# Optimization experiments

Hardware: AMD Instinct MI355X
Metric: run time of the kernel (lower is better)

The kernel has to match this reference:

```python
import jax, jax.numpy as jnp
import numpy as np

B, T, S, C, E, H = 4, 2048, 2048, 256, 512, 8
D = E // H
SCALE = E ** (-0.5)


def setup_inputs() -> dict:
    key = jax.random.key(0)
    ks = jax.random.split(key, 12)
    x = jax.random.normal(ks[0], (B, T, C), dtype=jnp.float32)
    context = jax.random.normal(ks[1], (B, S, E), dtype=jnp.float32)
    pad_mask = jax.random.randint(ks[2], (B, T, S), 0, 2) == 1
    p = 0.02
    # Conv1d kernel_size=1 weights stored squeezed: [out_ch, in_ch]
    w_in = jax.random.normal(ks[3], (E, C), dtype=jnp.float32) * p
    b_in = jnp.zeros((E,), dtype=jnp.float32)
    wq = jax.random.normal(ks[4], (E, E), dtype=jnp.float32) * p
    bq = jnp.zeros((E,), dtype=jnp.float32)
    wk = jax.random.normal(ks[5], (E, E), dtype=jnp.float32) * p
    bk = jnp.zeros((E,), dtype=jnp.float32)
    wv = jax.random.normal(ks[6], (E, E), dtype=jnp.float32) * p
    bv = jnp.zeros((E,), dtype=jnp.float32)
    w_out = jax.random.normal(ks[7], (C, E), dtype=jnp.float32) * p
    b_out = jnp.zeros((C,), dtype=jnp.float32)
    return {"x": x, "context": context, "pad_mask": pad_mask,
            "w_in": w_in, "b_in": b_in, "wq": wq, "bq": bq,
            "wk": wk, "bk": bk, "wv": wv, "bv": bv,
            "w_out": w_out, "b_out": b_out}


def reference(x, context, pad_mask, w_in, b_in, wq, bq, wk, bk, wv, bv, w_out, b_out):
    # proj_in: Conv1d k=1 == per-token linear on channel dim. [B,T,C] -> [B,T,E]
    xe = jnp.einsum('btc,ec->bte', x, w_in) + b_in
    Q = (xe @ wq.T + bq).reshape(B, T, H, D)       # query tokens
    K = (context @ wk.T + bk).reshape(B, S, H, D)  # key tokens
    V = (context @ wv.T + bv).reshape(B, S, H, D)
    att = jnp.einsum('bihd,bjhd->bhij', Q, K) * SCALE  # [B,H,T,S]
    att = jnp.where(pad_mask[:, None, :, :], jnp.float32(-1e9), att)
    att = jax.nn.softmax(att, axis=-1)
    out = jnp.einsum('bhij,bjhd->bihd', att, V).reshape(B, T, E)
    # proj_out: Conv1d k=1, [B,T,E] -> [B,T,C]
    out = jnp.einsum('bte,ce->btc', out, w_out) + b_out
    return out
```

## Files before the change

### kernel.cpp

```cpp
#include <hip/hip_runtime.h>
#include <cstdint>
#include <cstddef>

#define Bb 4
#define Tt 2048
#define Ssz 2048
#define Cc 256
#define Ee 512
#define Hh 8

typedef short bf8 __attribute__((ext_vector_type(8)));
typedef float f4 __attribute__((ext_vector_type(4)));
typedef float f16v __attribute__((ext_vector_type(16)));
typedef unsigned int u32x2 __attribute__((ext_vector_type(2)));
typedef unsigned int u32x4 __attribute__((ext_vector_type(4)));

__device__ __forceinline__ unsigned short f2bf(float x) {
  unsigned int u = __float_as_uint(x);
  u += 0x7fffu + ((u >> 16) & 1u);
  return (unsigned short)(u >> 16);
}

__device__ __forceinline__ bf8 cvt8(float4 a, float4 b) {
  bf8 r;
  r[0] = (short)f2bf(a.x); r[1] = (short)f2bf(a.y);
  r[2] = (short)f2bf(a.z); r[3] = (short)f2bf(a.w);
  r[4] = (short)f2bf(b.x); r[5] = (short)f2bf(b.y);
  r[6] = (short)f2bf(b.z); r[7] = (short)f2bf(b.w);
  return r;
}

#if __has_builtin(__builtin_amdgcn_perm)
#define PACK2(u0, u1) __builtin_amdgcn_perm((u1), (u0), 0x07060302u)
#else
#define PACK2(u0, u1) (((u0) >> 16) | ((u1) & 0xffff0000u))
#endif

#define EXPU(v) __float_as_uint(__builtin_amdgcn_exp2f(v))
#define MFMA32(a, b, c) __builtin_amdgcn_mfma_f32_32x32x16_bf16((a), (b), (c), 0, 0, 0)

__device__ __forceinline__ void pl32swap(unsigned int& a, unsigned int& b) {
#if __has_builtin(__builtin_amdgcn_permlane32_swap)
  u32x2 r = __builtin_amdgcn_permlane32_swap(a, b, false, false);
  a = r[0];
  b = r[1];
#else
  unsigned int ax = (unsigned int)__shfl_xor((int)a, 32);
  unsigned int bx = (unsigned int)__shfl_xor((int)b, 32);
  bool hi = (threadIdx.x & 32) != 0;
  unsigned int an = hi ? bx : a;
  unsigned int bn = hi ? b : ax;
  a = an;
  b = bn;
#endif
}

__global__ __launch_bounds__(256) void prep(const float* __restrict__ w_in,
                                            const float* __restrict__ b_in,
                                            const float* __restrict__ wq,
                                            const float* __restrict__ bq,
                                            const float* __restrict__ wk,
                                            const float* __restrict__ wv,
                                            const float* __restrict__ wo,
                                            unsigned short* __restrict__ wkvb,
                                            unsigned short* __restrict__ wob,
                                            unsigned short* __restrict__ wqin,
                                            float* __restrict__ bqinb, float qsc) {
  __shared__ unsigned short sh[128][72];
  const int bid = blockIdx.x, tid = threadIdx.x;
  if (bid < 512) {
    int i = bid * 256 + tid;
    const float* s = (i < 65536) ? wk : wv;
    int off = (i < 65536) ? i : i - 65536;
    float4 v = ((const float4*)s)[off];
    ushort4 o;
    o.x = f2bf(v.x); o.y = f2bf(v.y); o.z = f2bf(v.z); o.w = f2bf(v.w);
    ((ushort4*)wkvb)[i] = o;
  } else if (bid < 640) {
    int i = (bid - 512) * 256 + tid;
    float4 v = ((const float4*)wo)[i];
    ushort4 o;
    o.x = f2bf(v.x); o.y = f2bf(v.y); o.z = f2bf(v.z); o.w = f2bf(v.w);
    ((ushort4*)wob)[i] = o;
  } else if (bid < 672) {
    const int idx = bid - 640;
    const int m0 = (idx & 7) * 64, n0 = (idx >> 3) * 64;
    unsigned short (*As)[72] = (unsigned short (*)[72]) & sh[0][0];
    unsigned short (*Bs)[72] = (unsigned short (*)[72]) & sh[64][0];
    const int wave = tid >> 6, lane = tid & 63;
    const int lrow = lane & 15, quad = lane >> 4;
    const int wm = (wave >> 1) * 32, wn = (wave & 1) * 32;
    const int arow = tid >> 3, ac = tid & 7;
    f4 acc[2][2];
#pragma unroll
    for (int i = 0; i < 2; i++)
#pragma unroll
      for (int j = 0; j < 2; j++) {
        f4 z = {0.f, 0.f, 0.f, 0.f};
        acc[i][j] = z;
      }
    for (int kt = 0; kt < 8; kt++) {
#pragma unroll
      for (int i = 0; i < 2; i++) {
        int row = arow + i * 32;
        const float* src = wq + (size_t)(m0 + row) * Ee + kt * 64 + ac * 8;
        float4 v0 = *(const float4*)src, v1 = *(const float4*)(src + 4);
        bf8 av;
        av[0] = (short)f2bf(v0.x * qsc); av[1] = (short)f2bf(v0.y * qsc);
        av[2] = (short)f2bf(v0.z * qsc); av[3] = (short)f2bf(v0.w * qsc);
        av[4] = (short)f2bf(v1.x * qsc); av[5] = (short)f2bf(v1.y * qsc);
        av[6] = (short)f2bf(v1.z * qsc); av[7] = (short)f2bf(v1.w * qsc);
        *(bf8*)&As[row][ac * 8] = av;
        int c = n0 + row;
        bf8 bv;
#pragma unroll
        for (int k = 0; k < 8; k++)
          bv[k] = (short)f2bf(w_in[(size_t)(kt * 64 + ac * 8 + k) * Cc + c]);
        *(bf8*)&Bs[row][ac * 8] = bv;
      }
      __syncthreads();
#pragma unroll
      for (int kk = 0; kk < 2; kk++) {
        bf8 af[2], bff[2];
#pragma unroll
        for (int i = 0; i < 2; i++) af[i] = *(const bf8*)&As[wm + i * 16 + lrow][kk * 32 + quad * 8];
#pragma unroll
        for (int j = 0; j < 2; j++) bff[j] = *(const bf8*)&Bs[wn + j * 16 + lrow][kk * 32 + quad * 8];
#pragma unroll
        for (int i = 0; i < 2; i++)
#pragma unroll
          for (int j = 0; j < 2; j++)
            acc[i][j] = __builtin_amdgcn_mfma_f32_16x16x32_bf16(af[i], bff[j], acc[i][j], 0, 0, 0);
      }
      __syncthreads();
    }
#pragma unroll
    for (int j = 0; j < 2; j++)
#pragma unroll
      for (int i = 0; i < 2; i++)
#pragma unroll
        for (int r = 0; r < 4; r++)
          wqin[(size_t)(m0 + wm + i * 16 + quad * 4 + r) * Cc + n0 + wn + j * 16 + lrow] =
              f2bf(acc[i][j][r]);
  } else {
    const int o = (bid - 672) * 32 + (tid >> 3);
    const int k0 = (tid & 7) * 64;
    float s = 0.f;
#pragma unroll
    for (int i = 0; i < 16; i++) {
      float4 w = *(const float4*)(wq + (size_t)o * Ee + k0 + i * 4);
      float4 bb = *(const float4*)(b_in + k0 + i * 4);
      s += w.x * bb.x + w.y * bb.y + w.z * bb.z + w.w * bb.w;
    }
    s += __shfl_xor(s, 1);
    s += __shfl_xor(s, 2);
    s += __shfl_xor(s, 4);
    if ((tid & 7) == 0) bqinb[o] = (s + bq[o]) * qsc;
  }
}

__global__ __launch_bounds__(256) void qkv(const float* __restrict__ x,
                                           const float* __restrict__ ctx,
                                           const unsigned short* __restrict__ wqin,
                                           const float* __restrict__ bqinb,
                                           const unsigned short* __restrict__ wkv,
                                           const float* __restrict__ bk,
                                           const float* __restrict__ bv,
                                           unsigned short* __restrict__ Qb,
                                           unsigned short* __restrict__ Kf,
                                           unsigned short* __restrict__ Vf,
                                           const int* __restrict__ mask,
                                           unsigned int* __restrict__ mp) {
  __shared__ unsigned short As[128][72];
  __shared__ unsigned short Bs[128][72];
  const int bid = blockIdx.x, tid = threadIdx.x;
  if (bid >= 768) {
    int i = (bid - 768) * 256 + tid;
    const int4* src = (const int4*)mask + (size_t)i * 8;
    unsigned int w = 0;
#pragma unroll
    for (int k = 0; k < 8; k++) {
      int4 v = src[k];
      w |= (unsigned int)(v.x != 0) << (k * 4);
      w |= (unsigned int)(v.y != 0) << (k * 4 + 1);
      w |= (unsigned int)(v.z != 0) << (k * 4 + 2);
      w |= (unsigned int)(v.w != 0) << (k * 4 + 3);
    }
    mp[i] = w;
    return;
  }
  const bool isQ = bid < 256;
  const int idx = isQ ? bid : bid - 256;
  const int m0 = (idx & 63) * 128;
  const int n0 = (idx >> 6) * 128;
  const int K = isQ ? 256 : 512;
  const float* A = isQ ? x : ctx;
  const unsigned short* Bt = isQ ? wqin : wkv;

  const int wave = tid >> 6, lane = tid & 63;
  const int lrow = lane & 15, quad = lane >> 4;
  const int wm = (wave >> 1) * 64, wn = (wave & 1) * 64;
  const int arow = tid >> 3, ac = tid & 7;

  f4 acc[4][4];
#pragma unroll
  for (int i = 0; i < 4; i++)
#pragma unroll
    for (int j = 0; j < 4; j++) {
      f4 z = {0.f, 0.f, 0.f, 0.f};
      acc[i][j] = z;
    }

  float4 ap0[4], ap1[4];
  bf8 bpre[4];
#pragma unroll
  for (int i = 0; i < 4; i++) {
    const float* src = A + (size_t)(m0 + arow + i * 32) * K + ac * 8;
    ap0[i] = *(const float4*)src;
    ap1[i] = *(const float4*)(src + 4);
    bpre[i] = *(const bf8*)(Bt + (size_t)(n0 + arow + i * 32) * K + ac * 8);
  }

  const int nkt = K >> 6;
  for (int kt = 0; kt < nkt; ++kt) {
#pragma unroll
    for (int i = 0; i < 4; i++) {
      *(bf8*)&As[arow + i * 32][ac * 8] = cvt8(ap0[i], ap1[i]);
      *(bf8*)&Bs[arow + i * 32][ac * 8] = bpre[i];
    }
    __syncthreads();
    if (kt + 1 < nkt) {
      int k0 = (kt + 1) << 6;
#pragma unroll
      for (int i = 0; i < 4; i++) {
        const float* src = A + (size_t)(m0 + arow + i * 32) * K + k0 + ac * 8;
        ap0[i] = *(const float4*)src;
        ap1[i] = *(const float4*)(src + 4);
        bpre[i] = *(const bf8*)(Bt + (size_t)(n0 + arow + i * 32) * K + k0 + ac * 8);
      }
    }
#pragma unroll
    for (int kk = 0; kk < 2; kk++) {
      bf8 af[4], bff[4];
#pragma unroll
      for (int i = 0; i < 4; i++)
        af[i] = *(const bf8*)&As[wm + i * 16 + lrow][kk * 32 + quad * 8];
#pragma unroll
      for (int j = 0; j < 4; j++)
        bff[j] = *(const bf8*)&Bs[wn + j * 16 + lrow][kk * 32 + quad * 8];
#pragma unroll
      for (int i = 0; i < 4; i++)
#pragma unroll
        for (int j = 0; j < 4; j++)
          acc[i][j] = __builtin_amdgcn_mfma_f32_16x16x32_bf16(af[i], bff[j],
                                                              acc[i][j], 0, 0, 0);
    }
    __syncthreads();
  }

  if (isQ) {
#pragma unroll
    for (int j = 0; j < 4; j++) {
      int col = n0 + wn + j * 16 + lrow;
      float bvv = bqinb[col];
#pragma unroll
      for (int i = 0; i < 4; i++)
#pragma unroll
        for (int r = 0; r < 4; r++)
          Qb[(size_t)(m0 + wm + i * 16 + quad * 4 + r) * Ee + col] =
              f2bf(acc[i][j][r] + bvv);
    }
  } else if (n0 < 512) {
#pragma unroll
    for (int j = 0; j < 4; j++) {
      int col = n0 + wn + j * 16 + lrow;
      int h = col >> 6, dloc = col & 63;
      int cc = dloc >> 4, hh = (dloc >> 3) & 1, ee = dloc & 7;
      float bvv = bk[col];
#pragma unroll
      for (int i = 0; i < 4; i++)
#pragma unroll
        for (int r = 0; r < 4; r++) {
          int tok = m0 + wm + i * 16 + quad * 4 + r;
          int bb = tok >> 11, ss = tok & 2047;
          size_t addr = (((size_t)(bb * Hh + h) * 64 + (ss >> 5)) * 4 + cc) * 512 +
                        (hh * 32 + (ss & 31)) * 8 + ee;
          Kf[addr] = f2bf(acc[i][j][r] + bvv);
        }
    }
  } else {
#pragma unroll
    for (int j = 0; j < 4; j++) {
      int d = n0 - 512 + wn + j * 16 + lrow;
      int h = d >> 6, dd = d & 63;
      int l31 = dd & 31, dh = dd >> 5;
      float bvv = bv[d];
#pragma unroll
      for (int i = 0; i < 4; i++) {
        int tok = m0 + wm + i * 16 + quad * 4;
        int bb = tok >> 11, sl = tok & 2047;
        int stile = sl >> 6, cc = (sl >> 4) & 3, hh = (sl >> 3) & 1, e0 = sl & 7;
        ushort4 pk;
        pk.x = f2bf(acc[i][j][0] + bvv);
        pk.y = f2bf(acc[i][j][1] + bvv);
        pk.z = f2bf(acc[i][j][2] + bvv);
        pk.w = f2bf(acc[i][j][3] + bvv);
        size_t addr = ((((size_t)(bb * Hh + h) * 32 + stile) * 4 + cc) * 2 + dh) * 512 +
                      (hh * 32 + l31) * 8 + e0;
        *(ushort4*)(Vf + addr) = pk;
      }
    }
  }
}

template <bool OUT_BF16, int BM, int BN, int WGM>
__global__ __launch_bounds__(256) void gemm_bt(const unsigned short* __restrict__ A,
                                               const unsigned short* __restrict__ Bt,
                                               const float* __restrict__ bias0,
                                               void* __restrict__ Cout,
                                               int M, int N, int K) {
  constexpr int WGN = 4 / WGM;
  constexpr int MI = BM / (WGM * 16);
  constexpr int NJ = BN / (WGN * 16);
  constexpr int NA = BM / 32;
  constexpr int NB = BN / 32;
  __shared__ unsigned short As[BM][72];
  __shared__ unsigned short Bs[BN][72];
  const int tid = threadIdx.x;
  const int wave = tid >> 6, lane = tid & 63;
  const int lrow = lane & 15, quad = lane >> 4;
  const int wm = (wave / WGN) * (BM / WGM);
  const int wn = (wave % WGN) * (BN / WGN);
  const int m0 = blockIdx.x * BM, n0 = blockIdx.y * BN;
  const int arow = tid >> 3, ac = tid & 7;

  f4 acc[MI][NJ];
#pragma unroll
  for (int i = 0; i < MI; i++)
#pragma unroll
    for (int j = 0; j < NJ; j++) {
      f4 z = {0.f, 0.f, 0.f, 0.f};
      acc[i][j] = z;
    }

  bf8 apre[NA], bpre[NB];
#pragma unroll
  for (int i = 0; i < NA; i++)
    apre[i] = *(const bf8*)(A + (size_t)(m0 + arow + i * 32) * K + ac * 8);
#pragma unroll
  for (int i = 0; i < NB; i++)
    bpre[i] = *(const bf8*)(Bt + (size_t)(n0 + arow + i * 32) * K + ac * 8);

  const int nkt = K >> 6;
  for (int kt = 0; kt < nkt; ++kt) {
#pragma unroll
    for (int i = 0; i < NA; i++) *(bf8*)&As[arow + i * 32][ac * 8] = apre[i];
#pragma unroll
    for (int i = 0; i < NB; i++) *(bf8*)&Bs[arow + i * 32][ac * 8] = bpre[i];
    __syncthreads();
    if (kt + 1 < nkt) {
      int k0 = (kt + 1) << 6;
#pragma unroll
      for (int i = 0; i < NA; i++)
        apre[i] = *(const bf8*)(A + (size_t)(m0 + arow + i * 32) * K + k0 + ac * 8);
#pragma unroll
      for (int i = 0; i < NB; i++)
        bpre[i] = *(const bf8*)(Bt + (size_t)(n0 + arow + i * 32) * K + k0 + ac * 8);
    }
#pragma unroll
    for (int kk = 0; kk < 2; kk++) {
      bf8 af[MI], bff[NJ];
#pragma unroll
      for (int i = 0; i < MI; i++)
        af[i] = *(const bf8*)&As[wm + i * 16 + lrow][kk * 32 + quad * 8];
#pragma unroll
      for (int j = 0; j < NJ; j++)
        bff[j] = *(const bf8*)&Bs[wn + j * 16 + lrow][kk * 32 + quad * 8];
#pragma unroll
      for (int i = 0; i < MI; i++)
#pragma unroll
        for (int j = 0; j < NJ; j++)
          acc[i][j] = __builtin_amdgcn_mfma_f32_16x16x32_bf16(af[i], bff[j],
                                                              acc[i][j], 0, 0, 0);
    }
    __syncthreads();
  }

#pragma unroll
  for (int j = 0; j < NJ; j++) {
    int col = n0 + wn + j * 16 + lrow;
    float bvv = bias0 ? bias0[col] : 0.f;
#pragma unroll
    for (int i = 0; i < MI; i++) {
#pragma unroll
      for (int r = 0; r < 4; r++) {
        int row = m0 + wm + i * 16 + quad * 4 + r;
        float v = acc[i][j][r] + bvv;
        if (OUT_BF16)
          ((unsigned short*)Cout)[(size_t)row * N + col] = f2bf(v);
        else
          ((float*)Cout)[(size_t)row * N + col] = v;
      }
    }
  }
}

__global__ __launch_bounds__(256, 2) void attn(const unsigned short* __restrict__ Q,
                                               const unsigned short* __restrict__ Kf,
                                               const unsigned short* __restrict__ Vf,
                                               const unsigned int* __restrict__ mp,
                                               unsigned short* __restrict__ O) {
  const int tid = threadIdx.x;
  const int wave = tid >> 6, lane = tid & 63;
  const int l31 = lane & 31, hi = lane >> 5;
  const int bid = blockIdx.x;
  const int bh = bid & 31, b = bh >> 3, h = bh & 7;
  const int t0 = (bid >> 5) * 128;
  const int wm = wave * 32;

  const unsigned short* Qrow =
      Q + (size_t)(b * Tt + t0 + wm + l31) * Ee + h * 64 + hi * 8;
  bf8 qf[4];
#pragma unroll
  for (int c = 0; c < 4; c++) qf[c] = *(const bf8*)(Qrow + c * 16);

  f16v oacc0, oacc1, dacc;
#pragma unroll
  for (int r = 0; r < 16; r++) {
    oacc0[r] = 0.f;
    oacc1[r] = 0.f;
    dacc[r] = 0.f;
  }
  bf8 ones;
#pragma unroll
  for (int k = 0; k < 8; k++) ones[k] = (short)0x3F80;

  const unsigned short* Kl = Kf + (size_t)bh * 131072 + lane * 8;
  const unsigned short* Vl = Vf + (size_t)bh * 131072 + lane * 8;
  const unsigned int* mroww = mp + (size_t)(b * Tt + t0 + wm + l31) * 64;

  bf8 ka[2][4], kb[2][4];

  auto pfk = [&](bf8 (&KD)[2][4], int s0) {
#pragma unroll
    for (int sb = 0; sb < 2; sb++)
#pragma unroll
      for (int c = 0; c < 4; c++)
        KD[sb][c] = *(const bf8*)(Kl + (((((s0 >> 5) + sb) * 4) + c) << 9));
  };

  auto body = [&](bf8 (&KF)[2][4], bf8 (&KN)[2][4], int s0, bool dopf) {
    bf8 vf[4][2];
#pragma unroll
    for (int c = 0; c < 4; c++)
#pragma unroll
      for (int dh = 0; dh < 2; dh++)
        vf[c][dh] = *(const bf8*)(Vl + (((((s0 >> 6) * 4 + c) * 2) + dh) << 9));
    const uint2 mw = *(const uint2*)(mroww + (s0 >> 5));
    const unsigned int wsh0 = mw.x >> (4 * hi);
    const unsigned int wsh1 = mw.y >> (4 * hi);

    f16v sa0, sa1;
#pragma unroll
    for (int r = 0; r < 16; r++) {
      const int shft = (r & 3) + 8 * (r >> 2);
      sa0[r] = ((wsh0 >> shft) & 1u) ? -1e9f : 0.f;
      sa1[r] = ((wsh1 >> shft) & 1u) ? -1e9f : 0.f;
    }
    __builtin_amdgcn_s_setprio(1);
#pragma unroll
    for (int c = 0; c < 4; c++) {
      sa0 = MFMA32(KF[0][c], qf[c], sa0);
      sa1 = MFMA32(KF[1][c], qf[c], sa1);
    }
    __builtin_amdgcn_s_setprio(0);
    if (dopf) pfk(KN, s0 + 64);
    unsigned int X0[8], X1[8];
#pragma unroll
    for (int m = 0; m < 8; m++) {
      X0[m] = PACK2(EXPU(sa0[2 * m]), EXPU(sa0[2 * m + 1]));
      X1[m] = PACK2(EXPU(sa1[2 * m]), EXPU(sa1[2 * m + 1]));
    }
    __builtin_amdgcn_s_setprio(1);
#pragma unroll
    for (int c = 0; c < 4; c++) {
      const int m0 = 4 * (c & 1);
      unsigned int a0, a1, a2, a3;
      if (c < 2) {
        a0 = X0[m0]; a1 = X0[m0 + 1]; a2 = X0[m0 + 2]; a3 = X0[m0 + 3];
      } else {
        a0 = X1[m0]; a1 = X1[m0 + 1]; a2 = X1[m0 + 2]; a3 = X1[m0 + 3];
      }
      pl32swap(a0, a2);
      pl32swap(a1, a3);
      u32x4 pdv;
      pdv[0] = a0; pdv[1] = a1; pdv[2] = a2; pdv[3] = a3;
      bf8 pa = *(bf8*)&pdv;
      dacc = MFMA32(pa, ones, dacc);
      oacc0 = MFMA32(pa, vf[c][0], oacc0);
      oacc1 = MFMA32(pa, vf[c][1], oacc1);
    }
    __builtin_amdgcn_s_setprio(0);
  };

  pfk(ka, 0);
  for (int s0 = 0; s0 < Ssz; s0 += 128) {
    body(ka, kb, s0, true);
    body(kb, ka, s0 + 64, s0 + 128 < Ssz);
  }

#pragma unroll
  for (int r = 0; r < 16; r++) {
    const int tl = (r & 3) + 8 * (r >> 2) + 4 * hi;
    const float inv = 1.0f / dacc[r];
    const size_t off = (size_t)(b * Tt + t0 + wm + tl) * Ee + h * 64 + l31;
    O[off] = f2bf(oacc0[r] * inv);
    O[off + 32] = f2bf(oacc1[r] * inv);
  }
}

extern "C" void kernel_launch(void* const* d_in, const int* in_sizes, int n_in,
                              void* d_out, int out_size, void* d_ws, size_t ws_size,
                              hipStream_t stream) {
  const float* x    = (const float*)d_in[0];
  const float* ctx  = (const float*)d_in[1];
  const int*   mask = (const int*)d_in[2];
  const float* w_in = (const float*)d_in[3];
  const float* b_in = (const float*)d_in[4];
  const float* wq   = (const float*)d_in[5];
  const float* bq   = (const float*)d_in[6];
  const float* wk   = (const float*)d_in[7];
  const float* bk   = (const float*)d_in[8];
  const float* wv   = (const float*)d_in[9];
  const float* bv   = (const float*)d_in[10];
  const float* wo   = (const float*)d_in[11];
  const float* bo   = (const float*)d_in[12];

  const float qsc = 0.04419417382415922f * 1.4426950408889634f;

  unsigned short* ws = (unsigned short*)d_ws;
  unsigned int*   maskp = (unsigned int*)ws;
  unsigned short* wkvb  = ws + 1048576;
  unsigned short* wob   = ws + 1572864;
  unsigned short* wqin  = ws + 1703936;
  float*          bqinb = (float*)(ws + 1835008);
  unsigned short* Qb    = ws + 1836032;
  unsigned short* Kfb   = ws + 6030336;
  unsigned short* Vfb   = ws + 10224640;
  unsigned short* Ob    = ws + 14418944;

  prep<<<688, 256, 0, stream>>>(w_in, b_in, wq, bq, wk, wv, wo,
                                wkvb, wob, wqin, bqinb, qsc);
  qkv<<<2816, 256, 0, stream>>>(x, ctx, wqin, bqinb, wkvb, bk, bv, Qb, Kfb, Vfb,
                                mask, maskp);
  attn<<<512, 256, 0, stream>>>(Qb, Kfb, Vfb, maskp, Ob);
  gemm_bt<false, 64, 64, 2><<<dim3(128, 4), 256, 0, stream>>>(
      Ob, wob, bo, d_out, 8192, 256, 512);
}
```

Baseline: 230.4 us.

## Split attention key range across two wave groups and merge via shared memory

Doubles the attention block to 512 threads. Each group of four waves processes half of the key/value sequence for the same 128 query rows, and the partial numerators and denominators are combined through shared memory before normalization. This split-K scheme raises the number of active waves to hide memory and MFMA latency on a grid of only 512 blocks. In exchange it adds a 48KB shared buffer, a block barrier and a merge step. It also requests 4 blocks of 512 threads per CU, which may push register pressure up.

```diff
diff --git a/kernel.cpp b/kernel.cpp
--- a/kernel.cpp
+++ b/kernel.cpp
@@ -405,21 +405,24 @@
   }
 }
 
-__global__ __launch_bounds__(256, 2) void attn(const unsigned short* __restrict__ Q,
+__global__ __launch_bounds__(512, 4) void attn(const unsigned short* __restrict__ Q,
                                                const unsigned short* __restrict__ Kf,
                                                const unsigned short* __restrict__ Vf,
                                                const unsigned int* __restrict__ mp,
                                                unsigned short* __restrict__ O) {
+  __shared__ float mbuf[4][64][48];
   const int tid = threadIdx.x;
   const int wave = tid >> 6, lane = tid & 63;
   const int l31 = lane & 31, hi = lane >> 5;
+  const int wsub = wave & 3, shh = wave >> 2;
   const int bid = blockIdx.x;
   const int bh = bid & 31, b = bh >> 3, h = bh & 7;
   const int t0 = (bid >> 5) * 128;
-  const int wm = wave * 32;
+  const int tw = t0 + wsub * 32;
+  const int sbase = shh << 10;
 
   const unsigned short* Qrow =
-      Q + (size_t)(b * Tt + t0 + wm + l31) * Ee + h * 64 + hi * 8;
+      Q + (size_t)(b * Tt + tw + l31) * Ee + h * 64 + hi * 8;
   bf8 qf[4];
 #pragma unroll
   for (int c = 0; c < 4; c++) qf[c] = *(const bf8*)(Qrow + c * 16);
@@ -437,7 +440,7 @@
 
   const unsigned short* Kl = Kf + (size_t)bh * 131072 + lane * 8;
   const unsigned short* Vl = Vf + (size_t)bh * 131072 + lane * 8;
-  const unsigned int* mroww = mp + (size_t)(b * Tt + t0 + wm + l31) * 64;
+  const unsigned int* mroww = mp + (size_t)(b * Tt + tw + l31) * 64;
 
   bf8 ka[2][4], kb[2][4];
 
@@ -503,19 +506,33 @@
     __builtin_amdgcn_s_setprio(0);
   };
 
-  pfk(ka, 0);
-  for (int s0 = 0; s0 < Ssz; s0 += 128) {
+  pfk(ka, sbase);
+  for (int s0 = sbase; s0 < sbase + 1024; s0 += 128) {
     body(ka, kb, s0, true);
-    body(kb, ka, s0 + 64, s0 + 128 < Ssz);
-  }
-
-#pragma unroll
-  for (int r = 0; r < 16; r++) {
-    const int tl = (r & 3) + 8 * (r >> 2) + 4 * hi;
-    const float inv = 1.0f / dacc[r];
-    const size_t off = (size_t)(b * Tt + t0 + wm + tl) * Ee + h * 64 + l31;
-    O[off] = f2bf(oacc0[r] * inv);
-    O[off + 32] = f2bf(oacc1[r] * inv);
+    body(kb, ka, s0 + 64, s0 + 128 < sbase + 1024);
+  }
+
+  if (shh) {
+#pragma unroll
+    for (int q = 0; q < 4; q++) {
+      float4 v0 = {oacc0[4 * q], oacc0[4 * q + 1], oacc0[4 * q + 2], oacc0[4 * q + 3]};
+      float4 v1 = {oacc1[4 * q], oacc1[4 * q + 1], oacc1[4 * q + 2], oacc1[4 * q + 3]};
+      float4 v2 = {dacc[4 * q], dacc[4 * q + 1], dacc[4 * q + 2], dacc[4 * q + 3]};
+      *(float4*)&mbuf[wsub][lane][4 * q] = v0;
+      *(float4*)&mbuf[wsub][lane][16 + 4 * q] = v1;
+      *(float4*)&mbuf[wsub][lane][32 + 4 * q] = v2;
+    }
+  }
+  __syncthreads();
+  if (!shh) {
+#pragma unroll
+    for (int r = 0; r < 16; r++) {
+      const int tl = (r & 3) + 8 * (r >> 2) + 4 * hi;
+      const float inv = 1.0f / (dacc[r] + mbuf[wsub][lane][32 + r]);
+      const size_t off = (size_t)(b * Tt + tw + tl) * Ee + h * 64 + l31;
+      O[off] = f2bf((oacc0[r] + mbuf[wsub][lane][r]) * inv);
+      O[off + 32] = f2bf((oacc1[r] + mbuf[wsub][lane][16 + r]) * inv);
+    }
   }
 }
 
@@ -553,7 +570,7 @@
                                 wkvb, wob, wqin, bqinb, qsc);
   qkv<<<2816, 256, 0, stream>>>(x, ctx, wqin, bqinb, wkvb, bk, bv, Qb, Kfb, Vfb,
                                 mask, maskp);
-  attn<<<512, 256, 0, stream>>>(Qb, Kfb, Vfb, maskp, Ob);
+  attn<<<512, 512, 0, stream>>>(Qb, Kfb, Vfb, maskp, Ob);
   gemm_bt<false, 64, 64, 2><<<dim3(128, 4), 256, 0, stream>>>(
       Ob, wob, bo, d_out, 8192, 256, 512);
 }
```

After: 636.6 us. 2.76x slower.

## Software-pipeline QK MFMA of next tile behind PV MFMA of current tile

Applied to the files above, without the earlier changes.

Restructures the attention inner loop so the QK^T scores for the next 64-key tile are computed in the same MFMA burst as the PV accumulation of the current tile. The exp/pack work of one tile can then overlap matrix work from the neighbouring stage. The old double-buffered K register prefetch is replaced by a single K buffer loaded one iteration ahead. This holds the score accumulators across iterations, which raises register pressure, and the K load now has less time to complete before it is used.

```diff
diff --git a/kernel.cpp b/kernel.cpp
--- a/kernel.cpp
+++ b/kernel.cpp
@@ -439,49 +439,55 @@
   const unsigned short* Vl = Vf + (size_t)bh * 131072 + lane * 8;
   const unsigned int* mroww = mp + (size_t)(b * Tt + t0 + wm + l31) * 64;
 
-  bf8 ka[2][4], kb[2][4];
-
-  auto pfk = [&](bf8 (&KD)[2][4], int s0) {
-#pragma unroll
-    for (int sb = 0; sb < 2; sb++)
-#pragma unroll
-      for (int c = 0; c < 4; c++)
-        KD[sb][c] = *(const bf8*)(Kl + (((((s0 >> 5) + sb) * 4) + c) << 9));
-  };
-
-  auto body = [&](bf8 (&KF)[2][4], bf8 (&KN)[2][4], int s0, bool dopf) {
+  bf8 kf[2][4];
+  f16v sa0, sa1;
+
+#pragma unroll
+  for (int sb = 0; sb < 2; sb++)
+#pragma unroll
+    for (int c = 0; c < 4; c++)
+      kf[sb][c] = *(const bf8*)(Kl + ((size_t)(sb * 4 + c) << 9));
+  {
+    const uint2 mw = *(const uint2*)(mroww);
+    const unsigned int w0 = mw.x >> (4 * hi);
+    const unsigned int w1 = mw.y >> (4 * hi);
+#pragma unroll
+    for (int r = 0; r < 16; r++) {
+      const int sh = (r & 3) + 8 * (r >> 2);
+      sa0[r] = ((w0 >> sh) & 1u) ? -1e9f : 0.f;
+      sa1[r] = ((w1 >> sh) & 1u) ? -1e9f : 0.f;
+    }
+#pragma unroll
+    for (int c = 0; c < 4; c++) {
+      sa0 = MFMA32(kf[0][c], qf[c], sa0);
+      sa1 = MFMA32(kf[1][c], qf[c], sa1);
+    }
+  }
+
+  for (int n = 0; n < 32; n++) {
     bf8 vf[4][2];
 #pragma unroll
     for (int c = 0; c < 4; c++)
 #pragma unroll
       for (int dh = 0; dh < 2; dh++)
-        vf[c][dh] = *(const bf8*)(Vl + (((((s0 >> 6) * 4 + c) * 2) + dh) << 9));
-    const uint2 mw = *(const uint2*)(mroww + (s0 >> 5));
-    const unsigned int wsh0 = mw.x >> (4 * hi);
-    const unsigned int wsh1 = mw.y >> (4 * hi);
-
-    f16v sa0, sa1;
-#pragma unroll
-    for (int r = 0; r < 16; r++) {
-      const int shft = (r & 3) + 8 * (r >> 2);
-      sa0[r] = ((wsh0 >> shft) & 1u) ? -1e9f : 0.f;
-      sa1[r] = ((wsh1 >> shft) & 1u) ? -1e9f : 0.f;
-    }
-    __builtin_amdgcn_s_setprio(1);
-#pragma unroll
-    for (int c = 0; c < 4; c++) {
-      sa0 = MFMA32(KF[0][c], qf[c], sa0);
-      sa1 = MFMA32(KF[1][c], qf[c], sa1);
-    }
-    __builtin_amdgcn_s_setprio(0);
-    if (dopf) pfk(KN, s0 + 64);
+        vf[c][dh] = *(const bf8*)(Vl + ((size_t)((n * 4 + c) * 2 + dh) << 9));
+    const bool more = (n + 1 < 32);
+    uint2 mwn;
+    if (more) {
+#pragma unroll
+      for (int sb = 0; sb < 2; sb++)
+#pragma unroll
+        for (int c = 0; c < 4; c++)
+          kf[sb][c] = *(const bf8*)(Kl + ((size_t)((2 * (n + 1) + sb) * 4 + c) << 9));
+      mwn = *(const uint2*)(mroww + ((n + 1) << 1));
+    }
     unsigned int X0[8], X1[8];
 #pragma unroll
     for (int m = 0; m < 8; m++) {
       X0[m] = PACK2(EXPU(sa0[2 * m]), EXPU(sa0[2 * m + 1]));
       X1[m] = PACK2(EXPU(sa1[2 * m]), EXPU(sa1[2 * m + 1]));
     }
-    __builtin_amdgcn_s_setprio(1);
+    bf8 pa[4];
 #pragma unroll
     for (int c = 0; c < 4; c++) {
       const int m0 = 4 * (c & 1);
@@ -495,18 +501,33 @@
       pl32swap(a1, a3);
       u32x4 pdv;
       pdv[0] = a0; pdv[1] = a1; pdv[2] = a2; pdv[3] = a3;
-      bf8 pa = *(bf8*)&pdv;
-      dacc = MFMA32(pa, ones, dacc);
-      oacc0 = MFMA32(pa, vf[c][0], oacc0);
-      oacc1 = MFMA32(pa, vf[c][1], oacc1);
+      pa[c] = *(bf8*)&pdv;
+    }
+    if (more) {
+      const unsigned int w0 = mwn.x >> (4 * hi);
+      const unsigned int w1 = mwn.y >> (4 * hi);
+#pragma unroll
+      for (int r = 0; r < 16; r++) {
+        const int sh = (r & 3) + 8 * (r >> 2);
+        sa0[r] = ((w0 >> sh) & 1u) ? -1e9f : 0.f;
+        sa1[r] = ((w1 >> sh) & 1u) ? -1e9f : 0.f;
+      }
+    }
+    __builtin_amdgcn_s_setprio(1);
+#pragma unroll
+    for (int c = 0; c < 4; c++) {
+      dacc = MFMA32(pa[c], ones, dacc);
+      oacc0 = MFMA32(pa[c], vf[c][0], oacc0);
+      oacc1 = MFMA32(pa[c], vf[c][1], oacc1);
+    }
+    if (more) {
+#pragma unroll
+      for (int c = 0; c < 4; c++) {
+        sa0 = MFMA32(kf[0][c], qf[c], sa0);
+        sa1 = MFMA32(kf[1][c], qf[c], sa1);
+      }
     }
     __builtin_amdgcn_s_setprio(0);
-  };
-
-  pfk(ka, 0);
-  for (int s0 = 0; s0 < Ssz; s0 += 128) {
-    body(ka, kb, s0, true);
-    body(kb, ka, s0 + 64, s0 + 128 < Ssz);
   }
 
 #pragma unroll
```

New measurement: 240.9 us. 1.05x slower.
